# Optimization experiments

Measured on AMD Instinct MI355X. Metric: run time of the kernel, lower is better.

The kernel has to match this reference:

```python
import jax, jax.numpy as jnp
import numpy as np

QBITS = 8
QMIN, QMAX = -(2 ** (QBITS - 1)), 2 ** (QBITS - 1) - 1  # qint8: -128..127


def fq_act(x):
    """Per-tensor affine fake-quant (observer = min/max of tensor), with STE."""
    mn = jnp.minimum(jnp.min(x), 0.0)
    mx = jnp.maximum(jnp.max(x), 0.0)
    scale = jnp.maximum((mx - mn) / (QMAX - QMIN), 1e-8)
    zp = QMIN - jnp.round(mn / scale)
    q = jnp.clip(jnp.round(x / scale) + zp, QMIN, QMAX)
    y = (q - zp) * scale
    return x + jax.lax.stop_gradient(y - x)


def fq_w(w):
    """Per-tensor symmetric weight fake-quant, with STE."""
    scale = jnp.maximum(jnp.max(jnp.abs(w)) / QMAX, 1e-8)
    y = jnp.clip(jnp.round(w / scale), QMIN, QMAX) * scale
    return w + jax.lax.stop_gradient(y - w)


def setup_inputs() -> dict:
    key = jax.random.key(0)
    ks = jax.random.split(key, 8)
    B, T, F, K = 32, 1024, 512, 31
    return {
        "x": jax.random.normal(ks[0], (B, T, F), jnp.float32),
        "ln_scale": jnp.ones((F,), jnp.float32),
        "ln_bias": jnp.zeros((F,), jnp.float32),
        "w1": jax.random.normal(ks[1], (2 * F, F), jnp.float32) * 0.02,
        "b1": jax.random.normal(ks[2], (2 * F,), jnp.float32) * 0.02,
        "dw_w": jax.random.normal(ks[3], (F, 1, K), jnp.float32) * 0.1,
        "dw_b": jax.random.normal(ks[4], (F,), jnp.float32) * 0.02,
        "bn_gamma": jnp.ones((F,), jnp.float32),
        "bn_beta": jnp.zeros((F,), jnp.float32),
        "bn_mean": jnp.zeros((F,), jnp.float32),
        "bn_var": jax.random.uniform(ks[5], (F,), jnp.float32, 0.5, 1.5),
        "w2": jax.random.normal(ks[6], (F, F), jnp.float32) * 0.02,
        "b2": jax.random.normal(ks[7], (F,), jnp.float32) * 0.02,
    }


def reference(x, ln_scale, ln_bias, w1, b1, dw_w, dw_b,
              bn_gamma, bn_beta, bn_mean, bn_var, w2, b2):
    F = x.shape[-1]
    # --- custom L1 layer norm, fake-quant in/out ---
    t = fq_act(x)
    t = t - jnp.mean(t, axis=-1, keepdims=True)
    t = t / (jnp.sum(jnp.abs(t), axis=-1, keepdims=True) / F + 1e-5)
    t = t * ln_scale + ln_bias
    t = fq_act(t)
    # --- pointwise conv 1 (linear F -> 2F), quant-wrapped ---
    t = fq_act(t)
    t = jnp.einsum("btf,of->bto", t, fq_w(w1)) + b1
    t = fq_act(t)
    # --- GLU, quant-wrapped ---
    t = fq_act(t)
    a, g = jnp.split(t, 2, axis=-1)
    t = a * jax.nn.sigmoid(g)
    t = fq_act(t)
    # --- depthwise conv over time, quant-wrapped ---
    t = jnp.transpose(t, (0, 2, 1))  # [B,F,T]
    t = fq_act(t)
    t = jax.lax.conv_general_dilated(
        t, fq_w(dw_w), window_strides=(1,), padding=[((dw_w.shape[-1] - 1) // 2,) * 2],
        dimension_numbers=("NCH", "OIH", "NCH"), feature_group_count=F,
    ) + dw_b[:, None]
    t = fq_act(t)
    # --- batch norm (eval mode, running stats), quant-wrapped ---
    t = fq_act(t)
    t = (t - bn_mean[:, None]) * (bn_gamma[:, None] / jnp.sqrt(bn_var[:, None] + 1e-5)) + bn_beta[:, None]
    t = fq_act(t)
    t = jnp.transpose(t, (0, 2, 1))  # [B,T,F]
    # --- SiLU activation, quant-wrapped ---
    t = fq_act(t)
    t = jax.nn.silu(t)
    t = fq_act(t)
    # --- pointwise conv 2 (linear F -> F), quant-wrapped ---
    t = fq_act(t)
    t = jnp.einsum("btf,of->bto", t, fq_w(w2)) + b2
    t = fq_act(t)
    return t  # dropout is identity at eval
```

## Files before the change

kernel.cpp:

```cpp
#include <hip/hip_runtime.h>
#include <stdint.h>
#include <math.h>

#define INF __builtin_inff()

typedef __attribute__((ext_vector_type(4))) float f32x4;
typedef __attribute__((ext_vector_type(2))) float f32x2;
typedef __attribute__((ext_vector_type(8))) short s16x8;
typedef __attribute__((ext_vector_type(4))) short s16x4;

#define S_XMN 0
#define S_XMX 1
#define S_T1MN 2
#define S_T1MX 3
#define S_T4MN 4
#define S_T4MX 5
#define S_T7MN 6
#define S_T7MX 7
#define S_CVMN 8
#define S_CVMX 9
#define S_BNMN 10
#define S_BNMX 11
#define S_SIMN 12
#define S_SIMX 13
#define S_T18MN 14
#define S_T18MX 15
#define S_W1 16
#define S_W2 17
#define S_DW 18
#define NSLOT 19

#define NTOT 16777216L

__device__ __forceinline__ unsigned enc(float f) {
  unsigned u = __float_as_uint(f);
  return (u & 0x80000000u) ? ~u : (u | 0x80000000u);
}
__device__ __forceinline__ float dec(unsigned k) {
  return (k & 0x80000000u) ? __uint_as_float(k & 0x7FFFFFFFu) : __uint_as_float(~k);
}

struct FQ { float s, zp; };

__device__ __forceinline__ FQ fq_params(float mn_t, float mx_t) {
  float mn = fminf(mn_t, 0.0f), mx = fmaxf(mx_t, 0.0f);
  FQ p;
  p.s = fmaxf((mx - mn) / 255.0f, 1e-8f);
  p.zp = -128.0f - rintf(mn / p.s);
  return p;
}
__device__ __forceinline__ float fq_apply(float x, FQ p) {
  float q = rintf(x / p.s) + p.zp;
  q = fminf(fmaxf(q, -128.0f), 127.0f);
  return (q - p.zp) * p.s;
}
__device__ __forceinline__ float fq_qmz(float x, FQ p) {
  float q = rintf(x / p.s) + p.zp;
  q = fminf(fmaxf(q, -128.0f), 127.0f);
  return q - p.zp;
}
__device__ __forceinline__ void fq_pair(const unsigned* slots, int idx, FQ& p1, FQ& p2) {
  float mn = dec(slots[idx]), mx = dec(slots[idx + 1]);
  p1 = fq_params(mn, mx);
  float ymn = fq_apply(mn, p1), ymx = fq_apply(mx, p1);
  p2 = fq_params(ymn, ymx);
}
__device__ __forceinline__ unsigned short to_bf16(float v) {
  return (unsigned short)(__float_as_uint(v) >> 16);
}
__device__ __forceinline__ float from_bf16(unsigned short u) {
  return __uint_as_float(((unsigned)u) << 16);
}

__device__ __forceinline__ void mm_block_atomic(float mn, float mx, unsigned* smn, unsigned* smx) {
#pragma unroll
  for (int o = 32; o > 0; o >>= 1) {
    mn = fminf(mn, __shfl_down(mn, o, 64));
    mx = fmaxf(mx, __shfl_down(mx, o, 64));
  }
  __shared__ float rmn[16], rmx[16];
  int lane = threadIdx.x & 63, wid = threadIdx.x >> 6;
  int nw = blockDim.x >> 6;
  __syncthreads();
  if (lane == 0) { rmn[wid] = mn; rmx[wid] = mx; }
  __syncthreads();
  if (threadIdx.x == 0) {
    for (int i = 1; i < nw; ++i) { mn = fminf(mn, rmn[i]); mx = fmaxf(mx, rmx[i]); }
    atomicMin(smn, enc(mn));
    atomicMax(smx, enc(mx));
  }
}

__global__ void k_init(unsigned* __restrict__ slots, const float* __restrict__ gm,
                       const float* __restrict__ vr, float* __restrict__ gs) {
  int i = threadIdx.x;
  if (i < NSLOT) slots[i] = (i < 16) ? ((i & 1) ? enc(-INF) : enc(INF)) : enc(0.0f);
  gs[i] = gm[i] / sqrtf(vr[i] + 1e-5f);
}

__global__ __launch_bounds__(256) void k_redmm(const float* __restrict__ x, unsigned* __restrict__ slots) {
  long i = ((long)blockIdx.x * 256 + threadIdx.x) * 4;
  const long stride = (long)2048 * 256 * 4;
  float mn = INF, mx = -INF;
  for (; i < NTOT; i += stride) {
    f32x4 v = *(const f32x4*)(x + i);
    mn = fminf(mn, fminf(fminf(v.x, v.y), fminf(v.z, v.w)));
    mx = fmaxf(mx, fmaxf(fmaxf(v.x, v.y), fmaxf(v.z, v.w)));
  }
  mm_block_atomic(mn, mx, slots + S_XMN, slots + S_XMX);
}

__global__ __launch_bounds__(256) void k_wabs(const float* __restrict__ w1, const float* __restrict__ w2,
                                              const float* __restrict__ dw, unsigned* __restrict__ slots) {
  int b = blockIdx.x;
  const float* p; int slot; long base;
  if (b < 2048) { p = w1; slot = S_W1; base = (long)b * 256; }
  else if (b < 3072) { p = w2; slot = S_W2; base = (long)(b - 2048) * 256; }
  else { p = dw; slot = S_DW; base = (long)(b - 3072) * 256; }
  float v = fabsf(p[base + threadIdx.x]);
#pragma unroll
  for (int o = 32; o > 0; o >>= 1) v = fmaxf(v, __shfl_down(v, o, 64));
  __shared__ float r[4];
  int lane = threadIdx.x & 63, wid = threadIdx.x >> 6;
  if (lane == 0) r[wid] = v;
  __syncthreads();
  if (threadIdx.x == 0) {
    v = fmaxf(fmaxf(r[0], r[1]), fmaxf(r[2], r[3]));
    atomicMax(slots + slot, enc(v));
  }
}

__global__ __launch_bounds__(256) void k_wq(const float* __restrict__ w1, const float* __restrict__ w2,
    const float* __restrict__ dw, unsigned short* __restrict__ w1q, unsigned short* __restrict__ w2q,
    float* __restrict__ dwq, const unsigned* __restrict__ slots) {
  int b = blockIdx.x;
  if (b < 2048) {
    float s = fmaxf(dec(slots[S_W1]) / 127.0f, 1e-8f);
    long i = (long)b * 256 + threadIdx.x;
    float q = fminf(fmaxf(rintf(w1[i] / s), -128.0f), 127.0f);
    w1q[i] = to_bf16(q);
  } else if (b < 3072) {
    float s = fmaxf(dec(slots[S_W2]) / 127.0f, 1e-8f);
    long i = (long)(b - 2048) * 256 + threadIdx.x;
    float q = fminf(fmaxf(rintf(w2[i] / s), -128.0f), 127.0f);
    w2q[i] = to_bf16(q);
  } else {
    float s = fmaxf(dec(slots[S_DW]) / 127.0f, 1e-8f);
    long i = (long)(b - 3072) * 256 + threadIdx.x;
    float q = fminf(fmaxf(rintf(dw[i] / s), -128.0f), 127.0f);
    dwq[i] = q;
  }
}

__device__ __forceinline__ float block_sum256(float v, float* sh) {
#pragma unroll
  for (int o = 32; o > 0; o >>= 1) v += __shfl_down(v, o, 64);
  int lane = threadIdx.x & 63, wid = threadIdx.x >> 6;
  __syncthreads();
  if (lane == 0) sh[wid] = v;
  __syncthreads();
  return sh[0] + sh[1] + sh[2] + sh[3];
}

__device__ __forceinline__ f32x2 ln_row(const float* __restrict__ xr, int c, FQ p0,
                                        f32x2 sc, f32x2 bi, float* sh) {
  f32x2 xv = *(const f32x2*)(xr + c);
  float a0 = fq_apply(xv.x, p0), a1 = fq_apply(xv.y, p0);
  float mean = block_sum256(a0 + a1, sh) / 512.0f;
  a0 -= mean; a1 -= mean;
  float denom = block_sum256(fabsf(a0) + fabsf(a1), sh) / 512.0f + 1e-5f;
  f32x2 o;
  o.x = (a0 / denom) * sc.x + bi.x;
  o.y = (a1 / denom) * sc.y + bi.y;
  return o;
}

__global__ __launch_bounds__(256) void k_lnmm(const float* __restrict__ x, const float* __restrict__ lns,
    const float* __restrict__ lnb, unsigned* __restrict__ slots) {
  __shared__ float sh[4];
  FQ p0 = fq_params(dec(slots[S_XMN]), dec(slots[S_XMX]));
  int c = threadIdx.x * 2;
  f32x2 sc = *(const f32x2*)(lns + c);
  f32x2 bi = *(const f32x2*)(lnb + c);
  float lmn = INF, lmx = -INF;
  for (int rr = 0; rr < 16; ++rr) {
    long row = (long)blockIdx.x * 16 + rr;
    f32x2 a = ln_row(x + row * 512, c, p0, sc, bi, sh);
    lmn = fminf(lmn, fminf(a.x, a.y));
    lmx = fmaxf(lmx, fmaxf(a.x, a.y));
  }
  mm_block_atomic(lmn, lmx, slots + S_T1MN, slots + S_T1MX);
}

__global__ __launch_bounds__(256) void k_qa(const float* __restrict__ x, const float* __restrict__ lns,
    const float* __restrict__ lnb, unsigned short* __restrict__ A1, const unsigned* __restrict__ slots) {
  __shared__ float sh[4];
  FQ p0 = fq_params(dec(slots[S_XMN]), dec(slots[S_XMX]));
  FQ p1, p2; fq_pair(slots, S_T1MN, p1, p2);
  int c = threadIdx.x * 2;
  f32x2 sc = *(const f32x2*)(lns + c);
  f32x2 bi = *(const f32x2*)(lnb + c);
  for (int rr = 0; rr < 16; ++rr) {
    long row = (long)blockIdx.x * 16 + rr;
    f32x2 a = ln_row(x + row * 512, c, p0, sc, bi, sh);
    unsigned pk = (unsigned)to_bf16(fq_qmz(fq_apply(a.x, p1), p2))
                | ((unsigned)to_bf16(fq_qmz(fq_apply(a.y, p1), p2)) << 16);
    *(unsigned*)(A1 + row * 512 + c) = pk;
  }
}

__global__ __launch_bounds__(256) void k_gemm(const unsigned short* __restrict__ A,
    const unsigned short* __restrict__ Bm, const float* __restrict__ bias,
    float* __restrict__ C, int N, unsigned* __restrict__ slots, int mmIdx, int wIdx, int omIdx) {
  __shared__ __align__(16) unsigned short lA[128 * 64];
  __shared__ __align__(16) unsigned short lB[128 * 64];
  FQ p1, p2; fq_pair(slots, mmIdx, p1, p2);
  float sw = fmaxf(dec(slots[wIdx]) / 127.0f, 1e-8f);
  float sAB = p2.s * sw;
  int tid = threadIdx.x;
  int m0 = blockIdx.y * 128, n0 = blockIdx.x * 128;
  int lane = tid & 63, wid = tid >> 6;
  int wm = (wid >> 1) * 64, wn = (wid & 1) * 64;
  const f32x4 fz = {0.0f, 0.0f, 0.0f, 0.0f};
  f32x4 acc[4][4];
#pragma unroll
  for (int mi = 0; mi < 4; ++mi)
#pragma unroll
    for (int ni = 0; ni < 4; ++ni) acc[mi][ni] = fz;
  int sr = tid >> 1;
  int scu = (tid & 1) * 32;
  int swz = (sr & 7) * 8;
  const unsigned short* Ag = A + (long)(m0 + sr) * 512 + scu;
  const unsigned short* Bg = Bm + (long)(n0 + sr) * 512 + scu;
  int fr = lane & 15;
  int fc = (lane >> 4) * 8;
  for (int kt = 0; kt < 8; ++kt) {
    s16x8 ra[4], rb[4];
#pragma unroll
    for (int j = 0; j < 4; ++j) {
      ra[j] = *(const s16x8*)(Ag + kt * 64 + j * 8);
      rb[j] = *(const s16x8*)(Bg + kt * 64 + j * 8);
    }
    __syncthreads();
#pragma unroll
    for (int j = 0; j < 4; ++j) {
      *(s16x8*)&lA[sr * 64 + ((scu + j * 8) ^ swz)] = ra[j];
      *(s16x8*)&lB[sr * 64 + ((scu + j * 8) ^ swz)] = rb[j];
    }
    __syncthreads();
#pragma unroll
    for (int ks = 0; ks < 2; ++ks) {
      s16x8 af[4], bfv[4];
#pragma unroll
      for (int mi = 0; mi < 4; ++mi) {
        int r = wm + mi * 16 + fr;
        af[mi] = *(const s16x8*)&lA[r * 64 + ((ks * 32 + fc) ^ ((r & 7) * 8))];
      }
#pragma unroll
      for (int ni = 0; ni < 4; ++ni) {
        int r = wn + ni * 16 + fr;
        bfv[ni] = *(const s16x8*)&lB[r * 64 + ((ks * 32 + fc) ^ ((r & 7) * 8))];
      }
#pragma unroll
      for (int mi = 0; mi < 4; ++mi)
#pragma unroll
        for (int ni = 0; ni < 4; ++ni)
          acc[mi][ni] = __builtin_amdgcn_mfma_f32_16x16x32_bf16(af[mi], bfv[ni], acc[mi][ni], 0, 0, 0);
    }
  }
  float lmn = INF, lmx = -INF;
  int rb0 = m0 + wm + ((lane >> 4) << 2);
  int cb0 = n0 + wn + (lane & 15);
#pragma unroll
  for (int mi = 0; mi < 4; ++mi) {
#pragma unroll
    for (int ni = 0; ni < 4; ++ni) {
      int col = cb0 + ni * 16;
      float bv = bias[col];
#pragma unroll
      for (int r = 0; r < 4; ++r) {
        int rowi = rb0 + mi * 16 + r;
        float v = sAB * acc[mi][ni][r] + bv;
        C[(long)rowi * N + col] = v;
        lmn = fminf(lmn, v); lmx = fmaxf(lmx, v);
      }
    }
  }
  mm_block_atomic(lmn, lmx, slots + omIdx, slots + omIdx + 1);
}

__global__ __launch_bounds__(256) void k_glu(const float* __restrict__ t4, float* __restrict__ t7,
                                             unsigned* __restrict__ slots) {
  FQ p1, p2; fq_pair(slots, S_T4MN, p1, p2);
  long i = ((long)blockIdx.x * 256 + threadIdx.x) * 4;
  const long stride = (long)2048 * 256 * 4;
  float lmn = INF, lmx = -INF;
  for (; i < NTOT; i += stride) {
    long r = i >> 9;
    int c = (int)(i & 511);
    const float* pa = t4 + r * 1024 + c;
    f32x4 av = *(const f32x4*)pa;
    f32x4 gv = *(const f32x4*)(pa + 512);
    f32x4 o;
#pragma unroll
    for (int j = 0; j < 4; ++j) {
      float a = fq_apply(fq_apply(av[j], p1), p2);
      float g = fq_apply(fq_apply(gv[j], p1), p2);
      float y = a * (1.0f / (1.0f + expf(-g)));
      o[j] = y;
      lmn = fminf(lmn, y); lmx = fmaxf(lmx, y);
    }
    *(f32x4*)(t7 + i) = o;
  }
  mm_block_atomic(lmn, lmx, slots + S_T7MN, slots + S_T7MX);
}

__global__ __launch_bounds__(256) void k_conv(const float* __restrict__ t7,
    const float* __restrict__ dwq, const float* __restrict__ dwb,
    float* __restrict__ out, unsigned* __restrict__ slots) {
  FQ p1, p2; fq_pair(slots, S_T7MN, p1, p2);
  float sdw = fmaxf(dec(slots[S_DW]) / 127.0f, 1e-8f);
  float scv = p2.s * sdw;
  int t0 = blockIdx.x * 32;
  int f = blockIdx.y * 256 + threadIdx.x;
  int b = blockIdx.z;
  const float* base = t7 + (long)b * 1024 * 512 + f;
  float col[62];
#pragma unroll
  for (int r = 0; r < 62; ++r) {
    int t = t0 - 15 + r;
    float q = 0.0f;
    if ((unsigned)t < 1024u) q = fq_qmz(fq_apply(base[(long)t * 512], p1), p2);
    col[r] = q;
  }
  float w31[31];
#pragma unroll
  for (int k = 0; k < 31; ++k) w31[k] = dwq[f * 31 + k];
  float bias = dwb[f];
  float* orow = out + ((long)b * 1024 + t0) * 512 + f;
  float lmn = INF, lmx = -INF;
#pragma unroll
  for (int j = 0; j < 32; ++j) {
    float acc = 0.0f;
#pragma unroll
    for (int k = 0; k < 31; ++k) acc += col[j + k] * w31[k];
    float v = scv * acc + bias;
    lmn = fminf(lmn, v); lmx = fmaxf(lmx, v);
    orow[(long)j * 512] = v;
  }
  mm_block_atomic(lmn, lmx, slots + S_CVMN, slots + S_CVMX);
}

__device__ __forceinline__ float bn_val(float v, FQ c1, FQ c2, float gsv, float muv, float btv) {
  float y = fq_apply(fq_apply(v, c1), c2);
  return (y - muv) * gsv + btv;
}

__global__ __launch_bounds__(256) void k_bnmm(const float* __restrict__ conv,
    const float* __restrict__ gs, const float* __restrict__ mu, const float* __restrict__ bt,
    unsigned* __restrict__ slots) {
  FQ c1, c2; fq_pair(slots, S_CVMN, c1, c2);
  long i = ((long)blockIdx.x * 256 + threadIdx.x) * 4;
  const long stride = (long)2048 * 256 * 4;
  float lmn = INF, lmx = -INF;
  for (; i < NTOT; i += stride) {
    int f0 = (int)(i & 511);
    f32x4 v = *(const f32x4*)(conv + i);
    f32x4 g4 = *(const f32x4*)(gs + f0);
    f32x4 m4 = *(const f32x4*)(mu + f0);
    f32x4 b4 = *(const f32x4*)(bt + f0);
#pragma unroll
    for (int j = 0; j < 4; ++j) {
      float r2 = bn_val(v[j], c1, c2, g4[j], m4[j], b4[j]);
      lmn = fminf(lmn, r2); lmx = fmaxf(lmx, r2);
    }
  }
  mm_block_atomic(lmn, lmx, slots + S_BNMN, slots + S_BNMX);
}

__global__ __launch_bounds__(256) void k_silumm(const float* __restrict__ conv,
    const float* __restrict__ gs, const float* __restrict__ mu, const float* __restrict__ bt,
    unsigned* __restrict__ slots) {
  FQ c1, c2; fq_pair(slots, S_CVMN, c1, c2);
  FQ b1q, b2q; fq_pair(slots, S_BNMN, b1q, b2q);
  long i = ((long)blockIdx.x * 256 + threadIdx.x) * 4;
  const long stride = (long)2048 * 256 * 4;
  float lmn = INF, lmx = -INF;
  for (; i < NTOT; i += stride) {
    int f0 = (int)(i & 511);
    f32x4 v = *(const f32x4*)(conv + i);
    f32x4 g4 = *(const f32x4*)(gs + f0);
    f32x4 m4 = *(const f32x4*)(mu + f0);
    f32x4 b4 = *(const f32x4*)(bt + f0);
#pragma unroll
    for (int j = 0; j < 4; ++j) {
      float z = fq_apply(fq_apply(bn_val(v[j], c1, c2, g4[j], m4[j], b4[j]), b1q), b2q);
      float si = z * (1.0f / (1.0f + expf(-z)));
      lmn = fminf(lmn, si); lmx = fmaxf(lmx, si);
    }
  }
  mm_block_atomic(lmn, lmx, slots + S_SIMN, slots + S_SIMX);
}

__global__ __launch_bounds__(256) void k_q2(const float* __restrict__ conv,
    const float* __restrict__ gs, const float* __restrict__ mu, const float* __restrict__ bt,
    unsigned short* __restrict__ A2, const unsigned* __restrict__ slots) {
  FQ c1, c2; fq_pair(slots, S_CVMN, c1, c2);
  FQ b1q, b2q; fq_pair(slots, S_BNMN, b1q, b2q);
  FQ s1, s2; fq_pair(slots, S_SIMN, s1, s2);
  long i = ((long)blockIdx.x * 256 + threadIdx.x) * 4;
  const long stride = (long)2048 * 256 * 4;
  for (; i < NTOT; i += stride) {
    int f0 = (int)(i & 511);
    f32x4 v = *(const f32x4*)(conv + i);
    f32x4 g4 = *(const f32x4*)(gs + f0);
    f32x4 m4 = *(const f32x4*)(mu + f0);
    f32x4 b4 = *(const f32x4*)(bt + f0);
    s16x4 o;
#pragma unroll
    for (int j = 0; j < 4; ++j) {
      float z = fq_apply(fq_apply(bn_val(v[j], c1, c2, g4[j], m4[j], b4[j]), b1q), b2q);
      float si = z * (1.0f / (1.0f + expf(-z)));
      o[j] = (short)to_bf16(fq_qmz(fq_apply(si, s1), s2));
    }
    *(s16x4*)(A2 + i) = o;
  }
}

__global__ __launch_bounds__(256) void k_final(const float* __restrict__ t18, float* __restrict__ out,
                                               const unsigned* __restrict__ slots) {
  FQ p = fq_params(dec(slots[S_T18MN]), dec(slots[S_T18MX]));
  long i = ((long)blockIdx.x * 256 + threadIdx.x) * 4;
  const long stride = (long)2048 * 256 * 4;
  for (; i < NTOT; i += stride) {
    f32x4 v = *(const f32x4*)(t18 + i);
    f32x4 o;
#pragma unroll
    for (int j = 0; j < 4; ++j) o[j] = fq_apply(v[j], p);
    *(f32x4*)(out + i) = o;
  }
}

extern "C" void kernel_launch(void* const* d_in, const int* in_sizes, int n_in,
                              void* d_out, int out_size, void* d_ws, size_t ws_size,
                              hipStream_t stream) {
  const float* x   = (const float*)d_in[0];
  const float* lns = (const float*)d_in[1];
  const float* lnb = (const float*)d_in[2];
  const float* w1  = (const float*)d_in[3];
  const float* b1  = (const float*)d_in[4];
  const float* dw  = (const float*)d_in[5];
  const float* dwb = (const float*)d_in[6];
  const float* gm  = (const float*)d_in[7];
  const float* bt  = (const float*)d_in[8];
  const float* mu  = (const float*)d_in[9];
  const float* vr  = (const float*)d_in[10];
  const float* w2  = (const float*)d_in[11];
  const float* b2  = (const float*)d_in[12];
  float* out = (float*)d_out;
  char* ws = (char*)d_ws;

  const size_t OFF_B = 134217728;
  const size_t OFF_D = OFF_B + 67108864;
  const size_t OFF_W = OFF_D + 33554432;
  const size_t NEED = OFF_W + 1048576 + 524288 + 63488 + 2048 + 256;
  if (ws_size < NEED) return;

  float* buf0 = (float*)ws;
  float* bufB = (float*)(ws + OFF_B);
  unsigned short* bufD = (unsigned short*)(ws + OFF_D);
  unsigned short* w1q = (unsigned short*)(ws + OFF_W);
  unsigned short* w2q = (unsigned short*)(ws + OFF_W + 1048576);
  float* dwq = (float*)(ws + OFF_W + 1048576 + 524288);
  float* gs  = (float*)(ws + OFF_W + 1048576 + 524288 + 63488);
  unsigned* slots = (unsigned*)(ws + OFF_W + 1048576 + 524288 + 63488 + 2048);

  k_init<<<1, 512, 0, stream>>>(slots, gm, vr, gs);
  k_redmm<<<2048, 256, 0, stream>>>(x, slots);
  k_wabs<<<3134, 256, 0, stream>>>(w1, w2, dw, slots);
  k_wq<<<3134, 256, 0, stream>>>(w1, w2, dw, w1q, w2q, dwq, slots);
  k_lnmm<<<2048, 256, 0, stream>>>(x, lns, lnb, slots);
  k_qa<<<2048, 256, 0, stream>>>(x, lns, lnb, bufD, slots);
  k_gemm<<<dim3(8, 256), 256, 0, stream>>>(bufD, w1q, b1, buf0, 1024, slots, S_T1MN, S_W1, S_T4MN);
  k_glu<<<2048, 256, 0, stream>>>(buf0, bufB, slots);
  k_conv<<<dim3(32, 2, 32), 256, 0, stream>>>(bufB, dwq, dwb, buf0, slots);
  k_bnmm<<<2048, 256, 0, stream>>>(buf0, gs, mu, bt, slots);
  k_silumm<<<2048, 256, 0, stream>>>(buf0, gs, mu, bt, slots);
  k_q2<<<2048, 256, 0, stream>>>(buf0, gs, mu, bt, bufD, slots);
  k_gemm<<<dim3(4, 256), 256, 0, stream>>>(bufD, w2q, b2, bufB, 512, slots, S_SIMN, S_W2, S_T18MN);
  k_final<<<2048, 256, 0, stream>>>(bufB, out, slots);
}
```

Baseline: 801.6 us.

## Quantize intermediates to int8 with LUT-based double fake-quant and wave-per-row layernorm

Layernorm now uses one wave per row with shuffle-only reductions, which removes block-level syncs. Chained double fake-quant steps are replaced by 256-entry shared-memory lookup tables indexed by the first quantization level. The GLU output and the conv output are stored as int8 codes (new k_qt7 pass, and a fused quantize-plus-BN min/max pass), so later passes read 1 byte instead of 4. The cost is an extra pass over t7 and some LUT setup with a syncthreads in every block.

```diff
diff --git a/kernel.cpp b/kernel.cpp
--- a/kernel.cpp
+++ b/kernel.cpp
@@ -5,9 +5,9 @@
 #define INF __builtin_inff()
 
 typedef __attribute__((ext_vector_type(4))) float f32x4;
-typedef __attribute__((ext_vector_type(2))) float f32x2;
 typedef __attribute__((ext_vector_type(8))) short s16x8;
 typedef __attribute__((ext_vector_type(4))) short s16x4;
+typedef __attribute__((ext_vector_type(4))) char c8x4;
 
 #define S_XMN 0
 #define S_XMX 1
@@ -59,6 +59,11 @@
   q = fminf(fmaxf(q, -128.0f), 127.0f);
   return q - p.zp;
 }
+__device__ __forceinline__ int qidx(float x, FQ p) {
+  float q = rintf(x / p.s) + p.zp;
+  q = fminf(fmaxf(q, -128.0f), 127.0f);
+  return (int)q + 128;
+}
 __device__ __forceinline__ void fq_pair(const unsigned* slots, int idx, FQ& p1, FQ& p2) {
   float mn = dec(slots[idx]), mx = dec(slots[idx + 1]);
   p1 = fq_params(mn, mx);
@@ -68,9 +73,6 @@
 __device__ __forceinline__ unsigned short to_bf16(float v) {
   return (unsigned short)(__float_as_uint(v) >> 16);
 }
-__device__ __forceinline__ float from_bf16(unsigned short u) {
-  return __uint_as_float(((unsigned)u) << 16);
-}
 
 __device__ __forceinline__ void mm_block_atomic(float mn, float mx, unsigned* smn, unsigned* smx) {
 #pragma unroll
@@ -89,6 +91,12 @@
     atomicMin(smn, enc(mn));
     atomicMax(smx, enc(mx));
   }
+}
+
+__device__ __forceinline__ float wave_sum(float v) {
+#pragma unroll
+  for (int o = 1; o < 64; o <<= 1) v += __shfl_xor(v, o, 64);
+  return v;
 }
 
 __global__ void k_init(unsigned* __restrict__ slots, const float* __restrict__ gm,
@@ -152,60 +160,80 @@
   }
 }
 
-__device__ __forceinline__ float block_sum256(float v, float* sh) {
-#pragma unroll
-  for (int o = 32; o > 0; o >>= 1) v += __shfl_down(v, o, 64);
-  int lane = threadIdx.x & 63, wid = threadIdx.x >> 6;
-  __syncthreads();
-  if (lane == 0) sh[wid] = v;
-  __syncthreads();
-  return sh[0] + sh[1] + sh[2] + sh[3];
-}
-
-__device__ __forceinline__ f32x2 ln_row(const float* __restrict__ xr, int c, FQ p0,
-                                        f32x2 sc, f32x2 bi, float* sh) {
-  f32x2 xv = *(const f32x2*)(xr + c);
-  float a0 = fq_apply(xv.x, p0), a1 = fq_apply(xv.y, p0);
-  float mean = block_sum256(a0 + a1, sh) / 512.0f;
-  a0 -= mean; a1 -= mean;
-  float denom = block_sum256(fabsf(a0) + fabsf(a1), sh) / 512.0f + 1e-5f;
-  f32x2 o;
-  o.x = (a0 / denom) * sc.x + bi.x;
-  o.y = (a1 / denom) * sc.y + bi.y;
-  return o;
+__device__ __forceinline__ void ln_row_wave(const float* __restrict__ xr, int lane, FQ p0,
+    const f32x4& sc0, const f32x4& sc1, const f32x4& bi0, const f32x4& bi1,
+    f32x4& o0, f32x4& o1) {
+  f32x4 v0 = *(const f32x4*)(xr + lane * 4);
+  f32x4 v1 = *(const f32x4*)(xr + 256 + lane * 4);
+  float a[8];
+#pragma unroll
+  for (int j = 0; j < 4; ++j) { a[j] = fq_apply(v0[j], p0); a[4 + j] = fq_apply(v1[j], p0); }
+  float s = a[0] + a[1] + a[2] + a[3] + a[4] + a[5] + a[6] + a[7];
+  float mean = wave_sum(s) / 512.0f;
+#pragma unroll
+  for (int j = 0; j < 8; ++j) a[j] -= mean;
+  float l1 = fabsf(a[0]) + fabsf(a[1]) + fabsf(a[2]) + fabsf(a[3])
+           + fabsf(a[4]) + fabsf(a[5]) + fabsf(a[6]) + fabsf(a[7]);
+  float denom = wave_sum(l1) / 512.0f + 1e-5f;
+#pragma unroll
+  for (int j = 0; j < 4; ++j) {
+    o0[j] = (a[j] / denom) * sc0[j] + bi0[j];
+    o1[j] = (a[4 + j] / denom) * sc1[j] + bi1[j];
+  }
 }
 
 __global__ __launch_bounds__(256) void k_lnmm(const float* __restrict__ x, const float* __restrict__ lns,
     const float* __restrict__ lnb, unsigned* __restrict__ slots) {
-  __shared__ float sh[4];
   FQ p0 = fq_params(dec(slots[S_XMN]), dec(slots[S_XMX]));
-  int c = threadIdx.x * 2;
-  f32x2 sc = *(const f32x2*)(lns + c);
-  f32x2 bi = *(const f32x2*)(lnb + c);
+  int lane = threadIdx.x & 63, wv = threadIdx.x >> 6;
+  long gw = (long)blockIdx.x * 4 + wv;
+  f32x4 sc0 = *(const f32x4*)(lns + lane * 4);
+  f32x4 sc1 = *(const f32x4*)(lns + 256 + lane * 4);
+  f32x4 bi0 = *(const f32x4*)(lnb + lane * 4);
+  f32x4 bi1 = *(const f32x4*)(lnb + 256 + lane * 4);
   float lmn = INF, lmx = -INF;
-  for (int rr = 0; rr < 16; ++rr) {
-    long row = (long)blockIdx.x * 16 + rr;
-    f32x2 a = ln_row(x + row * 512, c, p0, sc, bi, sh);
-    lmn = fminf(lmn, fminf(a.x, a.y));
-    lmx = fmaxf(lmx, fmaxf(a.x, a.y));
+  for (int r = 0; r < 4; ++r) {
+    long row = gw + (long)r * 8192;
+    f32x4 o0, o1;
+    ln_row_wave(x + row * 512, lane, p0, sc0, sc1, bi0, bi1, o0, o1);
+#pragma unroll
+    for (int j = 0; j < 4; ++j) {
+      lmn = fminf(lmn, fminf(o0[j], o1[j]));
+      lmx = fmaxf(lmx, fmaxf(o0[j], o1[j]));
+    }
   }
   mm_block_atomic(lmn, lmx, slots + S_T1MN, slots + S_T1MX);
 }
 
 __global__ __launch_bounds__(256) void k_qa(const float* __restrict__ x, const float* __restrict__ lns,
     const float* __restrict__ lnb, unsigned short* __restrict__ A1, const unsigned* __restrict__ slots) {
-  __shared__ float sh[4];
+  __shared__ unsigned short lut[256];
   FQ p0 = fq_params(dec(slots[S_XMN]), dec(slots[S_XMX]));
   FQ p1, p2; fq_pair(slots, S_T1MN, p1, p2);
-  int c = threadIdx.x * 2;
-  f32x2 sc = *(const f32x2*)(lns + c);
-  f32x2 bi = *(const f32x2*)(lnb + c);
-  for (int rr = 0; rr < 16; ++rr) {
-    long row = (long)blockIdx.x * 16 + rr;
-    f32x2 a = ln_row(x + row * 512, c, p0, sc, bi, sh);
-    unsigned pk = (unsigned)to_bf16(fq_qmz(fq_apply(a.x, p1), p2))
-                | ((unsigned)to_bf16(fq_qmz(fq_apply(a.y, p1), p2)) << 16);
-    *(unsigned*)(A1 + row * 512 + c) = pk;
+  {
+    int i = threadIdx.x;
+    float y1 = ((float)(i - 128) - p1.zp) * p1.s;
+    lut[i] = to_bf16(fq_qmz(y1, p2));
+  }
+  __syncthreads();
+  int lane = threadIdx.x & 63, wv = threadIdx.x >> 6;
+  long gw = (long)blockIdx.x * 4 + wv;
+  f32x4 sc0 = *(const f32x4*)(lns + lane * 4);
+  f32x4 sc1 = *(const f32x4*)(lns + 256 + lane * 4);
+  f32x4 bi0 = *(const f32x4*)(lnb + lane * 4);
+  f32x4 bi1 = *(const f32x4*)(lnb + 256 + lane * 4);
+  for (int r = 0; r < 4; ++r) {
+    long row = gw + (long)r * 8192;
+    f32x4 o0, o1;
+    ln_row_wave(x + row * 512, lane, p0, sc0, sc1, bi0, bi1, o0, o1);
+    s16x4 q0, q1;
+#pragma unroll
+    for (int j = 0; j < 4; ++j) {
+      q0[j] = (short)lut[qidx(o0[j], p1)];
+      q1[j] = (short)lut[qidx(o1[j], p1)];
+    }
+    *(s16x4*)(A1 + row * 512 + lane * 4) = q0;
+    *(s16x4*)(A1 + row * 512 + 256 + lane * 4) = q1;
   }
 }
 
@@ -291,7 +319,14 @@
 
 __global__ __launch_bounds__(256) void k_glu(const float* __restrict__ t4, float* __restrict__ t7,
                                              unsigned* __restrict__ slots) {
+  __shared__ float lut[256];
   FQ p1, p2; fq_pair(slots, S_T4MN, p1, p2);
+  {
+    int i = threadIdx.x;
+    float y1 = ((float)(i - 128) - p1.zp) * p1.s;
+    lut[i] = fq_apply(y1, p2);
+  }
+  __syncthreads();
   long i = ((long)blockIdx.x * 256 + threadIdx.x) * 4;
   const long stride = (long)2048 * 256 * 4;
   float lmn = INF, lmx = -INF;
@@ -304,8 +339,8 @@
     f32x4 o;
 #pragma unroll
     for (int j = 0; j < 4; ++j) {
-      float a = fq_apply(fq_apply(av[j], p1), p2);
-      float g = fq_apply(fq_apply(gv[j], p1), p2);
+      float a = lut[qidx(av[j], p1)];
+      float g = lut[qidx(gv[j], p1)];
       float y = a * (1.0f / (1.0f + expf(-g)));
       o[j] = y;
       lmn = fminf(lmn, y); lmx = fmaxf(lmx, y);
@@ -315,22 +350,45 @@
   mm_block_atomic(lmn, lmx, slots + S_T7MN, slots + S_T7MX);
 }
 
-__global__ __launch_bounds__(256) void k_conv(const float* __restrict__ t7,
+__global__ __launch_bounds__(256) void k_qt7(const float* __restrict__ t7, signed char* __restrict__ q7,
+                                             const unsigned* __restrict__ slots) {
+  __shared__ signed char lutq[256];
+  FQ p1, p2; fq_pair(slots, S_T7MN, p1, p2);
+  {
+    int i = threadIdx.x;
+    float y1 = ((float)(i - 128) - p1.zp) * p1.s;
+    float q = fminf(fmaxf(rintf(y1 / p2.s) + p2.zp, -128.0f), 127.0f);
+    lutq[i] = (signed char)(int)q;
+  }
+  __syncthreads();
+  long i = ((long)blockIdx.x * 256 + threadIdx.x) * 4;
+  const long stride = (long)2048 * 256 * 4;
+  for (; i < NTOT; i += stride) {
+    f32x4 v = *(const f32x4*)(t7 + i);
+    c8x4 o;
+#pragma unroll
+    for (int j = 0; j < 4; ++j) o[j] = lutq[qidx(v[j], p1)];
+    *(c8x4*)(q7 + i) = o;
+  }
+}
+
+__global__ __launch_bounds__(256) void k_conv(const signed char* __restrict__ q7,
     const float* __restrict__ dwq, const float* __restrict__ dwb,
     float* __restrict__ out, unsigned* __restrict__ slots) {
   FQ p1, p2; fq_pair(slots, S_T7MN, p1, p2);
   float sdw = fmaxf(dec(slots[S_DW]) / 127.0f, 1e-8f);
   float scv = p2.s * sdw;
+  float zp2 = p2.zp;
   int t0 = blockIdx.x * 32;
   int f = blockIdx.y * 256 + threadIdx.x;
   int b = blockIdx.z;
-  const float* base = t7 + (long)b * 1024 * 512 + f;
+  const signed char* base = q7 + (long)b * 1024 * 512 + f;
   float col[62];
 #pragma unroll
   for (int r = 0; r < 62; ++r) {
     int t = t0 - 15 + r;
     float q = 0.0f;
-    if ((unsigned)t < 1024u) q = fq_qmz(fq_apply(base[(long)t * 512], p1), p2);
+    if ((unsigned)t < 1024u) q = (float)(int)base[(long)t * 512] - zp2;
     col[r] = q;
   }
   float w31[31];
@@ -351,15 +409,19 @@
   mm_block_atomic(lmn, lmx, slots + S_CVMN, slots + S_CVMX);
 }
 
-__device__ __forceinline__ float bn_val(float v, FQ c1, FQ c2, float gsv, float muv, float btv) {
-  float y = fq_apply(fq_apply(v, c1), c2);
-  return (y - muv) * gsv + btv;
-}
-
-__global__ __launch_bounds__(256) void k_bnmm(const float* __restrict__ conv,
-    const float* __restrict__ gs, const float* __restrict__ mu, const float* __restrict__ bt,
-    unsigned* __restrict__ slots) {
-  FQ c1, c2; fq_pair(slots, S_CVMN, c1, c2);
+__global__ __launch_bounds__(256) void k_qcv_bnmm(const float* __restrict__ conv,
+    signed char* __restrict__ qcv, const float* __restrict__ gs, const float* __restrict__ mu,
+    const float* __restrict__ bt, unsigned* __restrict__ slots) {
+  __shared__ signed char lutq[256];
+  FQ p1, p2; fq_pair(slots, S_CVMN, p1, p2);
+  {
+    int i = threadIdx.x;
+    float y1 = ((float)(i - 128) - p1.zp) * p1.s;
+    float q = fminf(fmaxf(rintf(y1 / p2.s) + p2.zp, -128.0f), 127.0f);
+    lutq[i] = (signed char)(int)q;
+  }
+  __syncthreads();
+  float s2 = p2.s, zp2 = p2.zp;
   long i = ((long)blockIdx.x * 256 + threadIdx.x) * 4;
   const long stride = (long)2048 * 256 * 4;
   float lmn = INF, lmx = -INF;
@@ -369,59 +431,87 @@
     f32x4 g4 = *(const f32x4*)(gs + f0);
     f32x4 m4 = *(const f32x4*)(mu + f0);
     f32x4 b4 = *(const f32x4*)(bt + f0);
-#pragma unroll
-    for (int j = 0; j < 4; ++j) {
-      float r2 = bn_val(v[j], c1, c2, g4[j], m4[j], b4[j]);
-      lmn = fminf(lmn, r2); lmx = fmaxf(lmx, r2);
-    }
+    c8x4 o;
+#pragma unroll
+    for (int j = 0; j < 4; ++j) {
+      signed char qc = lutq[qidx(v[j], p1)];
+      o[j] = qc;
+      float y2 = ((float)(int)qc - zp2) * s2;
+      float z = (y2 - m4[j]) * g4[j] + b4[j];
+      lmn = fminf(lmn, z); lmx = fmaxf(lmx, z);
+    }
+    *(c8x4*)(qcv + i) = o;
   }
   mm_block_atomic(lmn, lmx, slots + S_BNMN, slots + S_BNMX);
 }
 
-__global__ __launch_bounds__(256) void k_silumm(const float* __restrict__ conv,
+__global__ __launch_bounds__(256) void k_silumm(const signed char* __restrict__ qcv,
     const float* __restrict__ gs, const float* __restrict__ mu, const float* __restrict__ bt,
     unsigned* __restrict__ slots) {
+  __shared__ float lutb[256];
   FQ c1, c2; fq_pair(slots, S_CVMN, c1, c2);
   FQ b1q, b2q; fq_pair(slots, S_BNMN, b1q, b2q);
+  {
+    int i = threadIdx.x;
+    float y1 = ((float)(i - 128) - b1q.zp) * b1q.s;
+    lutb[i] = fq_apply(y1, b2q);
+  }
+  __syncthreads();
+  float s2 = c2.s, zp2 = c2.zp;
   long i = ((long)blockIdx.x * 256 + threadIdx.x) * 4;
   const long stride = (long)2048 * 256 * 4;
   float lmn = INF, lmx = -INF;
   for (; i < NTOT; i += stride) {
     int f0 = (int)(i & 511);
-    f32x4 v = *(const f32x4*)(conv + i);
+    c8x4 qv = *(const c8x4*)(qcv + i);
     f32x4 g4 = *(const f32x4*)(gs + f0);
     f32x4 m4 = *(const f32x4*)(mu + f0);
     f32x4 b4 = *(const f32x4*)(bt + f0);
 #pragma unroll
     for (int j = 0; j < 4; ++j) {
-      float z = fq_apply(fq_apply(bn_val(v[j], c1, c2, g4[j], m4[j], b4[j]), b1q), b2q);
-      float si = z * (1.0f / (1.0f + expf(-z)));
+      float y2 = ((float)(int)qv[j] - zp2) * s2;
+      float z = (y2 - m4[j]) * g4[j] + b4[j];
+      float z2 = lutb[qidx(z, b1q)];
+      float si = z2 * (1.0f / (1.0f + expf(-z2)));
       lmn = fminf(lmn, si); lmx = fmaxf(lmx, si);
     }
   }
   mm_block_atomic(lmn, lmx, slots + S_SIMN, slots + S_SIMX);
 }
 
-__global__ __launch_bounds__(256) void k_q2(const float* __restrict__ conv,
+__global__ __launch_bounds__(256) void k_q2(const signed char* __restrict__ qcv,
     const float* __restrict__ gs, const float* __restrict__ mu, const float* __restrict__ bt,
     unsigned short* __restrict__ A2, const unsigned* __restrict__ slots) {
+  __shared__ float lutb[256];
+  __shared__ unsigned short luts[256];
   FQ c1, c2; fq_pair(slots, S_CVMN, c1, c2);
   FQ b1q, b2q; fq_pair(slots, S_BNMN, b1q, b2q);
-  FQ s1, s2; fq_pair(slots, S_SIMN, s1, s2);
+  FQ s1q, s2q; fq_pair(slots, S_SIMN, s1q, s2q);
+  {
+    int i = threadIdx.x;
+    float yb = ((float)(i - 128) - b1q.zp) * b1q.s;
+    lutb[i] = fq_apply(yb, b2q);
+    float ys = ((float)(i - 128) - s1q.zp) * s1q.s;
+    luts[i] = to_bf16(fq_qmz(ys, s2q));
+  }
+  __syncthreads();
+  float s2 = c2.s, zp2 = c2.zp;
   long i = ((long)blockIdx.x * 256 + threadIdx.x) * 4;
   const long stride = (long)2048 * 256 * 4;
   for (; i < NTOT; i += stride) {
     int f0 = (int)(i & 511);
-    f32x4 v = *(const f32x4*)(conv + i);
+    c8x4 qv = *(const c8x4*)(qcv + i);
     f32x4 g4 = *(const f32x4*)(gs + f0);
     f32x4 m4 = *(const f32x4*)(mu + f0);
     f32x4 b4 = *(const f32x4*)(bt + f0);
     s16x4 o;
 #pragma unroll
     for (int j = 0; j < 4; ++j) {
-      float z = fq_apply(fq_apply(bn_val(v[j], c1, c2, g4[j], m4[j], b4[j]), b1q), b2q);
-      float si = z * (1.0f / (1.0f + expf(-z)));
-      o[j] = (short)to_bf16(fq_qmz(fq_apply(si, s1), s2));
+      float y2 = ((float)(int)qv[j] - zp2) * s2;
+      float z = (y2 - m4[j]) * g4[j] + b4[j];
+      float z2 = lutb[qidx(z, b1q)];
+      float si = z2 * (1.0f / (1.0f + expf(-z2)));
+      o[j] = (short)luts[qidx(si, s1q)];
     }
     *(s16x4*)(A2 + i) = o;
   }
@@ -469,6 +559,9 @@
   float* buf0 = (float*)ws;
   float* bufB = (float*)(ws + OFF_B);
   unsigned short* bufD = (unsigned short*)(ws + OFF_D);
+  signed char* q7  = (signed char*)(ws + OFF_D);
+  signed char* qcv = (signed char*)(ws + OFF_D + 16777216);
+  unsigned short* A2 = (unsigned short*)ws;
   unsigned short* w1q = (unsigned short*)(ws + OFF_W);
   unsigned short* w2q = (unsigned short*)(ws + OFF_W + 1048576);
   float* dwq = (float*)(ws + OFF_W + 1048576 + 524288);
@@ -476,17 +569,18 @@
   unsigned* slots = (unsigned*)(ws + OFF_W + 1048576 + 524288 + 63488 + 2048);
 
   k_init<<<1, 512, 0, stream>>>(slots, gm, vr, gs);
-  k_redmm<<<2048, 256, 0, stream>>>(x, slots);
   k_wabs<<<3134, 256, 0, stream>>>(w1, w2, dw, slots);
   k_wq<<<3134, 256, 0, stream>>>(w1, w2, dw, w1q, w2q, dwq, slots);
+  k_redmm<<<2048, 256, 0, stream>>>(x, slots);
   k_lnmm<<<2048, 256, 0, stream>>>(x, lns, lnb, slots);
   k_qa<<<2048, 256, 0, stream>>>(x, lns, lnb, bufD, slots);
   k_gemm<<<dim3(8, 256), 256, 0, stream>>>(bufD, w1q, b1, buf0, 1024, slots, S_T1MN, S_W1, S_T4MN);
   k_glu<<<2048, 256, 0, stream>>>(buf0, bufB, slots);
-  k_conv<<<dim3(32, 2, 32), 256, 0, stream>>>(bufB, dwq, dwb, buf0, slots);
-  k_bnmm<<<2048, 256, 0, stream>>>(buf0, gs, mu, bt, slots);
-  k_silumm<<<2048, 256, 0, stream>>>(buf0, gs, mu, bt, slots);
-  k_q2<<<2048, 256, 0, stream>>>(buf0, gs, mu, bt, bufD, slots);
-  k_gemm<<<dim3(4, 256), 256, 0, stream>>>(bufD, w2q, b2, bufB, 512, slots, S_SIMN, S_W2, S_T18MN);
+  k_qt7<<<2048, 256, 0, stream>>>(bufB, q7, slots);
+  k_conv<<<dim3(32, 2, 32), 256, 0, stream>>>(q7, dwq, dwb, buf0, slots);
+  k_qcv_bnmm<<<2048, 256, 0, stream>>>(buf0, qcv, gs, mu, bt, slots);
+  k_silumm<<<2048, 256, 0, stream>>>(qcv, gs, mu, bt, slots);
+  k_q2<<<2048, 256, 0, stream>>>(qcv, gs, mu, bt, A2, slots);
+  k_gemm<<<dim3(4, 256), 256, 0, stream>>>(A2, w2q, b2, bufB, 512, slots, S_SIMN, S_W2, S_T18MN);
   k_final<<<2048, 256, 0, stream>>>(bufB, out, slots);
 }
```

Result: faster. 748.7 us (-6.6%).
